# Optimization experiments

Hardware: AMD Instinct MI355X
Metric: run time of the kernel (lower is better)

The kernel has to match this reference:

```python
import jax, jax.numpy as jnp
import numpy as np

B, S, BD, AD, H, NITER = 16, 512, 768, 768, 12, 3  # batch, seq, bert_dim, attention_dim, heads, c_c_Attention_num
DH = AD // H
SCALE = float(np.sqrt(BD))  # note: original scales by sqrt(bert_dim), not head dim


def setup_inputs() -> dict:
    key = jax.random.key(0)
    ks = jax.random.split(key, 12)
    sd = 0.02
    return {
        "sequence1": jax.random.normal(ks[0], (B, S, BD), dtype=jnp.float32),
        "sequence2": jax.random.normal(ks[1], (B, S, BD), dtype=jnp.float32),
        # first-layer projections (bias=False), torch Linear weight layout [out, in]
        "Wq": jax.random.normal(ks[2], (AD, BD), dtype=jnp.float32) * sd,
        "Wk": jax.random.normal(ks[3], (AD, BD), dtype=jnp.float32) * sd,
        "Wv": jax.random.normal(ks[4], (AD, BD), dtype=jnp.float32) * sd,
        # later-layer projections (with bias), stacked over layer_num-1 = 2 layers
        "Wq1": jax.random.normal(ks[5], (2, AD, AD), dtype=jnp.float32) * sd,
        "bq1": jax.random.normal(ks[6], (2, AD), dtype=jnp.float32) * sd,
        "Wk1": jax.random.normal(ks[7], (2, AD, AD), dtype=jnp.float32) * sd,
        "bk1": jax.random.normal(ks[8], (2, AD), dtype=jnp.float32) * sd,
        "Wv1": jax.random.normal(ks[9], (2, AD, AD), dtype=jnp.float32) * sd,
        "bv1": jax.random.normal(ks[10], (2, AD), dtype=jnp.float32) * sd,
    }


def _attention(s1, s2, Wq, bq, Wk, bk, Wv, bv):
    # dropout is identity in eval mode
    q = s1 @ Wq.T + bq  # [B,S,AD]
    k = s2 @ Wk.T + bk
    v = s2 @ Wv.T + bv
    # torch.split along feature dim then stack on dim 0 == reshape to heads
    qh = q.reshape(B, S, H, DH)
    kh = k.reshape(B, S, H, DH)
    vh = v.reshape(B, S, H, DH)
    scores = jnp.einsum("bqhd,bkhd->hbqk", qh, kh)  # [H,B,S,S]
    scores = jax.nn.softmax(jnp.tanh(scores) / SCALE, axis=3)
    ctx = jnp.einsum("hbqk,bkhd->bqhd", scores, vh).reshape(B, S, AD)
    return ctx, scores


def reference(sequence1, sequence2, Wq, Wk, Wv, Wq1, bq1, Wk1, bk1, Wv1, bv1):
    s1, s2 = sequence1, sequence2
    ctx, sc = None, None
    for i in range(NITER):
        if i == 0:
            ctx, sc = _attention(s1, s2, Wq, 0.0, Wk, 0.0, Wv, 0.0)
        else:
            j = i - 1
            ctx, sc = _attention(s1, s2, Wq1[j], bq1[j], Wk1[j], bk1[j], Wv1[j], bv1[j])
        s1 = ctx
        s2 = ctx
    return ctx, ctx, sc
```

## Files before the change

### kernel.cpp

```cpp
#include <hip/hip_runtime.h>
#include <stdint.h>

typedef unsigned short u16;
typedef unsigned int u32;

typedef __bf16 bf16x8 __attribute__((ext_vector_type(8)));
typedef float f32x4 __attribute__((ext_vector_type(4)));

#define NQ 6291456
#define NW 589824
#define INV_SCALE 0.03608439182435161f
#define LOG2E2 2.885390081777927f

__device__ __forceinline__ u16 f2bf(float f) {
    u32 u = __float_as_uint(f);
    u32 r = (u + 0x7fffu + ((u >> 16) & 1u)) >> 16;
    return (u16)r;
}

__device__ __forceinline__ float score_p(float s) {
    float e  = exp2f(LOG2E2 * s);
    float th = 1.f - __fdividef(2.f, e + 1.f);
    float a  = th * INV_SCALE;
    return fmaf(a, fmaf(a, fmaf(a, 0.16666667f, 0.5f), 1.f), 1.f);
}

__device__ __forceinline__ void gload_lds16(const void* g, void* l) {
    __builtin_amdgcn_global_load_lds(
        (const __attribute__((address_space(1))) char*)(uintptr_t)g,
        (__attribute__((address_space(3))) char*)(uintptr_t)l, 16, 0, 0);
}

__device__ __forceinline__ f32x4 mfma16(bf16x8 a, bf16x8 b, f32x4 c) {
    return __builtin_amdgcn_mfma_f32_16x16x32_bf16(a, b, c, 0, 0, 0);
}

#define LDS_FENCE() asm volatile("s_waitcnt lgkmcnt(0)" ::: "memory")

struct CvtArgs {
    const float* src[8];
    u16* dst[8];
    int blk_start[8];
    int n4[8];
};

__global__ __launch_bounds__(256) void cvt_multi(CvtArgs a)
{
    const int bid = blockIdx.x;
    int seg = 0;
#pragma unroll
    for (int s = 1; s < 8; ++s) seg += (bid >= a.blk_start[s]);
    const int i = (bid - a.blk_start[seg]) * 256 + threadIdx.x;
    if (i < a.n4[seg]) {
        float4 v = ((const float4*)a.src[seg])[i];
        ushort4 o;
        o.x = f2bf(v.x); o.y = f2bf(v.y); o.z = f2bf(v.z); o.w = f2bf(v.w);
        ((ushort4*)a.dst[seg])[i] = o;
    }
}

__global__ __launch_bounds__(256, 2) void proj_gemm(
    const u16* __restrict__ A0, const u16* __restrict__ A1,
    const u16* __restrict__ Wq, const u16* __restrict__ Wk, const u16* __restrict__ Wv,
    const float* __restrict__ bq, const float* __restrict__ bk, const float* __restrict__ bv,
    u16* __restrict__ oq, u16* __restrict__ ok, u16* __restrict__ ov)
{
    __shared__ u16 sA[2][8192];
    __shared__ u16 sB[2][8192];

    const int z = blockIdx.z;
    const u16* A       = (z == 0) ? A0 : A1;
    const u16* W       = (z == 0) ? Wq : ((z == 1) ? Wk : Wv);
    const float* bias  = (z == 0) ? bq : ((z == 1) ? bk : bv);
    u16* out           = (z == 0) ? oq : ((z == 1) ? ok : ov);

    const int tid = threadIdx.x;
    const int wave = tid >> 6, lane = tid & 63;
    const int m0 = blockIdx.x * 128, n0 = blockIdx.y * 128;
    const int wrow = wave >> 1, wcol = wave & 1;
    const int lr = lane & 15, lg = lane >> 4;

    const int Lb0 = wave * 4096;
    const int srow = (Lb0 + lane * 16) >> 7;
    const int ssl = (lane & 7);

    f32x4 acc[4][4];
#pragma unroll
    for (int mi = 0; mi < 4; ++mi)
#pragma unroll
        for (int ni = 0; ni < 4; ++ni)
            acc[mi][ni] = (f32x4){0.f, 0.f, 0.f, 0.f};

#define STAGE(buf, k0)                                                          \
    {                                                                           \
        _Pragma("unroll")                                                       \
        for (int i = 0; i < 4; ++i) {                                           \
            const int row = srow + i * 8;                                       \
            const int sc16 = ssl ^ (row & 7);                                   \
            gload_lds16(A + (size_t)(m0 + row) * 768 + (k0) + sc16 * 8,         \
                        (char*)sA[buf] + Lb0 + i * 1024);                       \
            gload_lds16(W + (size_t)(n0 + row) * 768 + (k0) + sc16 * 8,         \
                        (char*)sB[buf] + Lb0 + i * 1024);                       \
        }                                                                       \
    }

    STAGE(0, 0);
    __syncthreads();

    for (int ks = 0; ks < 12; ++ks) {
        const int cur = ks & 1;
        if (ks < 11) STAGE(cur ^ 1, (ks + 1) * 64);
#pragma unroll
        for (int kk = 0; kk < 2; ++kk) {
            bf16x8 af[4], bfr[4];
#pragma unroll
            for (int t = 0; t < 4; ++t) {
                const int ar = wrow * 64 + t * 16 + lr;
                const int ac = (kk * 4 + lg) ^ (ar & 7);
                af[t] = *(const bf16x8*)((const char*)sA[cur] + ar * 128 + ac * 16);
                const int br = wcol * 64 + t * 16 + lr;
                const int bc = (kk * 4 + lg) ^ (br & 7);
                bfr[t] = *(const bf16x8*)((const char*)sB[cur] + br * 128 + bc * 16);
            }
#pragma unroll
            for (int mi = 0; mi < 4; ++mi)
#pragma unroll
                for (int ni = 0; ni < 4; ++ni)
                    acc[mi][ni] = mfma16(af[mi], bfr[ni], acc[mi][ni]);
        }
        __syncthreads();
    }
#undef STAGE

    float bvv[4] = {0.f, 0.f, 0.f, 0.f};
    if (bias) {
#pragma unroll
        for (int ni = 0; ni < 4; ++ni)
            bvv[ni] = bias[n0 + wcol * 64 + ni * 16 + lr];
    }
#pragma unroll
    for (int mi = 0; mi < 4; ++mi) {
#pragma unroll
        for (int ni = 0; ni < 4; ++ni) {
#pragma unroll
            for (int r = 0; r < 4; ++r) {
                const int rowM = m0 + wrow * 64 + mi * 16 + lg * 4 + r;
                const int colN = n0 + wcol * 64 + ni * 16 + lr;
                out[(size_t)rowM * 768 + colN] = f2bf(acc[mi][ni][r] + bvv[ni]);
            }
        }
    }
}

__global__ __launch_bounds__(256) void vtrans(const u16* __restrict__ v, u16* __restrict__ vT)
{
    __shared__ u16 t[64][80];
    const int blk = blockIdx.x;
    const int b = blk / 96, h = (blk / 8) % 12, st = blk & 7;
    const int tid = threadIdx.x;

    const u16* src = v + (size_t)(b * 512 + st * 64) * 768 + h * 64;
#pragma unroll
    for (int p = 0; p < 2; ++p) {
        const int srow = p * 32 + (tid >> 3), dp = tid & 7;
        uint4 d = *(const uint4*)(src + (size_t)srow * 768 + dp * 8);
        *(uint4*)&t[srow][dp * 8] = d;
    }
    __syncthreads();
    u16* dst = vT + (size_t)((b * 12 + h) * 64) * 512 + st * 64;
#pragma unroll
    for (int p = 0; p < 2; ++p) {
        const int drow = p * 32 + (tid >> 3), sp = tid & 7;
        union { u16 u[8]; uint4 v4; } o;
#pragma unroll
        for (int j = 0; j < 8; ++j) o.u[j] = t[sp * 8 + j][drow];
        *(uint4*)(dst + (size_t)drow * 512 + sp * 8) = o.v4;
    }
}

__global__ __launch_bounds__(256, 4) void attn_stream(
    const u16* __restrict__ q, const u16* __restrict__ k, const u16* __restrict__ vT,
    u16* __restrict__ ctx)
{
    __shared__ u16 sS[4][2][640];

    const int blk = blockIdx.x;
    const int b = blk / 96, h = (blk / 8) % 12, qc = blk & 7;
    const int tid = threadIdx.x, wave = tid >> 6, lane = tid & 63;
    const int q0 = qc * 64 + wave * 16;
    const int lr = lane & 15, lg = lane >> 4;

    const u16* qbase = q + (size_t)(b * 512 + q0 + lr) * 768 + h * 64 + lg * 8;
    bf16x8 aq0 = *(const bf16x8*)(qbase);
    bf16x8 aq1 = *(const bf16x8*)(qbase + 32);

    const u16* kbase = k + (size_t)(b * 512 + lr) * 768 + h * 64 + lg * 8;
    const u16* vbase = vT + (size_t)((b * 12 + h) * 64 + lr) * 512 + lg * 8;

    char* const myS0 = (char*)sS[wave][0];
    const int rdoff = lr * 80 + ((lg * 16) ^ ((lr & 3) << 4));

    float psum[4] = {0.f, 0.f, 0.f, 0.f};
    f32x4 o[4];
#pragma unroll
    for (int dt = 0; dt < 4; ++dt) o[dt] = (f32x4){0.f, 0.f, 0.f, 0.f};

    for (int w = 0; w < 16; ++w) {
        char* myS = myS0 + (w & 1) * 1280;
        const u16* kb = kbase + (size_t)w * 32 * 768;
        f32x4 s4a = (f32x4){0.f, 0.f, 0.f, 0.f};
        f32x4 s4b = (f32x4){0.f, 0.f, 0.f, 0.f};
        s4a = mfma16(aq0, *(const bf16x8*)kb, s4a);
        s4a = mfma16(aq1, *(const bf16x8*)(kb + 32), s4a);
        const u16* kb2 = kb + 16 * 768;
        s4b = mfma16(aq0, *(const bf16x8*)kb2, s4b);
        s4b = mfma16(aq1, *(const bf16x8*)(kb2 + 32), s4b);

#pragma unroll
        for (int c = 0; c < 2; ++c) {
#pragma unroll
            for (int r = 0; r < 4; ++r) {
                const float s = c ? s4b[r] : s4a[r];
                const float p = score_p(s);
                psum[r] += p;
                const int row = lg * 4 + r;
                const int byte = row * 80 + (((c * 16 + lr) * 2) ^ ((r & 3) << 4));
                *(u16*)(myS + byte) = f2bf(p);
            }
        }
        LDS_FENCE();
        bf16x8 pa = *(const bf16x8*)(myS + rdoff);
#pragma unroll
        for (int dt = 0; dt < 4; ++dt) {
            bf16x8 vb = *(const bf16x8*)(vbase + (size_t)dt * 16 * 512 + w * 32);
            o[dt] = mfma16(pa, vb, o[dt]);
        }
    }

#pragma unroll
    for (int r = 0; r < 4; ++r) {
        psum[r] += __shfl_xor(psum[r], 1);
        psum[r] += __shfl_xor(psum[r], 2);
        psum[r] += __shfl_xor(psum[r], 4);
        psum[r] += __shfl_xor(psum[r], 8);
    }
    float inv[4];
#pragma unroll
    for (int r = 0; r < 4; ++r) inv[r] = 1.f / psum[r];

#pragma unroll
    for (int dt = 0; dt < 4; ++dt) {
#pragma unroll
        for (int r = 0; r < 4; ++r) {
            const size_t gi = (size_t)(b * 512 + q0 + lg * 4 + r) * 768 + h * 64 + dt * 16 + lr;
            ctx[gi] = f2bf(o[dt][r] * inv[r]);
        }
    }
}

__global__ __launch_bounds__(256, 2) void attn_final(
    const u16* __restrict__ q, const u16* __restrict__ k, const u16* __restrict__ vT,
    float* __restrict__ ctxf, float* __restrict__ sc)
{
    __shared__ u16 sP[4][8192];
    __shared__ float ssum[4][16];

    const int blk = blockIdx.x;
    const int b = blk / 96, h = (blk / 8) % 12, qc = blk & 7;
    const int tid = threadIdx.x, wave = tid >> 6, lane = tid & 63;
    const int q0 = qc * 64 + wave * 16;
    const int lr = lane & 15, lg = lane >> 4;
    char* myP = (char*)sP[wave];

    const u16* qbase = q + (size_t)(b * 512 + q0 + lr) * 768 + h * 64 + lg * 8;
    bf16x8 aq0 = *(const bf16x8*)(qbase);
    bf16x8 aq1 = *(const bf16x8*)(qbase + 32);

    float psum[4] = {0.f, 0.f, 0.f, 0.f};
    const u16* kbase = k + (size_t)(b * 512 + lr) * 768 + h * 64 + lg * 8;

    for (int kt = 0; kt < 32; ++kt) {
        f32x4 s4 = (f32x4){0.f, 0.f, 0.f, 0.f};
        const u16* kb = kbase + (size_t)kt * 16 * 768;
        s4 = mfma16(aq0, *(const bf16x8*)kb, s4);
        s4 = mfma16(aq1, *(const bf16x8*)(kb + 32), s4);
#pragma unroll
        for (int r = 0; r < 4; ++r) {
            const int row = lg * 4 + r;
            const float p = score_p(s4[r]);
            psum[r] += p;
            const int byte = (row * 1024 + (kt * 16 + lr) * 2) ^ ((row & 7) << 4);
            *(u16*)(myP + byte) = f2bf(p);
        }
    }
#pragma unroll
    for (int r = 0; r < 4; ++r) {
        psum[r] += __shfl_xor(psum[r], 1);
        psum[r] += __shfl_xor(psum[r], 2);
        psum[r] += __shfl_xor(psum[r], 4);
        psum[r] += __shfl_xor(psum[r], 8);
    }
    float inv[4];
#pragma unroll
    for (int r = 0; r < 4; ++r) inv[r] = 1.f / psum[r];

    if (lr == 0) {
#pragma unroll
        for (int r = 0; r < 4; ++r) ssum[wave][lg * 4 + r] = inv[r];
    }

    const u16* vb0 = vT + (size_t)((b * 12 + h) * 64 + lr) * 512 + lg * 8;
#pragma unroll
    for (int dt = 0; dt < 4; ++dt) {
        f32x4 o = (f32x4){0.f, 0.f, 0.f, 0.f};
        const u16* vbb = vb0 + (size_t)dt * 16 * 512;
#pragma unroll
        for (int pk = 0; pk < 16; ++pk) {
            const int byte = (lr * 1024 + pk * 64 + lg * 16) ^ ((lr & 7) << 4);
            bf16x8 pa = *(const bf16x8*)(myP + byte);
            bf16x8 vb = *(const bf16x8*)(vbb + pk * 32);
            o = mfma16(pa, vb, o);
        }
#pragma unroll
        for (int r = 0; r < 4; ++r) {
            const float val = o[r] * inv[r];
            const size_t gi = (size_t)(b * 512 + q0 + lg * 4 + r) * 768 + h * 64 + dt * 16 + lr;
            ctxf[gi] = val;
            ctxf[gi + (size_t)NQ] = val;
        }
    }

#pragma unroll
    for (int row = 0; row < 16; ++row) {
        const float is = ssum[wave][row];
        const int byte = (row * 1024 + lane * 16) ^ ((row & 7) << 4);
        bf16x8 pv8 = *(const bf16x8*)(myP + byte);
        float4 o0, o1;
        o0.x = (float)pv8[0] * is; o0.y = (float)pv8[1] * is;
        o0.z = (float)pv8[2] * is; o0.w = (float)pv8[3] * is;
        o1.x = (float)pv8[4] * is; o1.y = (float)pv8[5] * is;
        o1.z = (float)pv8[6] * is; o1.w = (float)pv8[7] * is;
        float* dstp = sc + ((size_t)((h * 16 + b) * 512 + q0 + row)) * 512 + lane * 8;
        *(float4*)dstp = o0;
        *(float4*)(dstp + 4) = o1;
    }
}

extern "C" void kernel_launch(void* const* d_in, const int* in_sizes, int n_in,
                              void* d_out, int out_size, void* d_ws, size_t ws_size,
                              hipStream_t stream)
{
    if (n_in < 11) return;
    const float* seq1 = (const float*)d_in[0];
    const float* seq2 = (const float*)d_in[1];
    const float* Wq  = (const float*)d_in[2];
    const float* Wk  = (const float*)d_in[3];
    const float* Wv  = (const float*)d_in[4];
    const float* Wq1 = (const float*)d_in[5];
    const float* bq1 = (const float*)d_in[6];
    const float* Wk1 = (const float*)d_in[7];
    const float* bk1 = (const float*)d_in[8];
    const float* Wv1 = (const float*)d_in[9];
    const float* bv1 = (const float*)d_in[10];

    if (ws_size < ((size_t)7 * NQ + 9 * NW) * 2) return;
    u16* ws   = (u16*)d_ws;
    u16* q    = ws;
    u16* kk   = ws + (size_t)NQ;
    u16* vv   = ws + (size_t)2 * NQ;
    u16* vT   = ws + (size_t)3 * NQ;
    u16* ctx  = ws + (size_t)4 * NQ;
    u16* bs1  = ws + (size_t)5 * NQ;
    u16* bs2  = ws + (size_t)6 * NQ;
    u16* bWq  = ws + (size_t)7 * NQ;
    u16* bWk  = bWq  + (size_t)NW;
    u16* bWv  = bWk  + (size_t)NW;
    u16* bWq1 = bWv  + (size_t)NW;
    u16* bWk1 = bWq1 + (size_t)2 * NW;
    u16* bWv1 = bWk1 + (size_t)2 * NW;

    float* out = (float*)d_out;

    CvtArgs ca;
    const float* srcs[8] = {seq1, seq2, Wq, Wk, Wv, Wq1, Wk1, Wv1};
    u16* dsts[8] = {bs1, bs2, bWq, bWk, bWv, bWq1, bWk1, bWv1};
    const int n4s[8] = {NQ/4, NQ/4, NW/4, NW/4, NW/4, NW/2, NW/2, NW/2};
    int acc_blk = 0;
    for (int s = 0; s < 8; ++s) {
        ca.src[s] = srcs[s]; ca.dst[s] = dsts[s]; ca.n4[s] = n4s[s];
        ca.blk_start[s] = acc_blk;
        acc_blk += (n4s[s] + 255) / 256;
    }
    cvt_multi<<<acc_blk, 256, 0, stream>>>(ca);

    dim3 pgrid(64, 6, 3);

    proj_gemm<<<pgrid, 256, 0, stream>>>(bs1, bs2, bWq, bWk, bWv,
                                         nullptr, nullptr, nullptr, q, kk, vv);
    vtrans<<<1536, 256, 0, stream>>>(vv, vT);
    attn_stream<<<1536, 256, 0, stream>>>(q, kk, vT, ctx);

    proj_gemm<<<pgrid, 256, 0, stream>>>(ctx, ctx, bWq1, bWk1, bWv1,
                                         bq1, bk1, bv1, q, kk, vv);
    vtrans<<<1536, 256, 0, stream>>>(vv, vT);
    attn_stream<<<1536, 256, 0, stream>>>(q, kk, vT, ctx);

    proj_gemm<<<pgrid, 256, 0, stream>>>(ctx, ctx, bWq1 + (size_t)NW, bWk1 + (size_t)NW,
                                         bWv1 + (size_t)NW,
                                         bq1 + 768, bk1 + 768, bv1 + 768, q, kk, vv);
    vtrans<<<1536, 256, 0, stream>>>(vv, vT);
    attn_final<<<1536, 256, 0, stream>>>(q, kk, vT, out, out + (size_t)2 * NQ);
}
```

Before: 452.6 us.

## Recompute scores in two passes for final attention, streaming probabilities directly

The final attention kernel no longer holds the full 16x512 bf16 probability tile per wave in LDS. It makes one pass to get row sums, then a second pass that recomputes QK^T, writes the normalized fp32 scores straight to global memory, and streams P through a small double-buffered LDS tile into the PV MFMAs. This cuts LDS use enough to allow 4 blocks per SM, at the cost of recomputing the scores and tanh/exp. Both attention kernels also change block indexing so that consecutive blocks cover different batch-head pairs, which changes L2 locality. Scores are now written as 16-lane scalar rows instead of float4 vectors, which may hurt write coalescing.

```diff
diff --git a/kernel.cpp b/kernel.cpp
--- a/kernel.cpp
+++ b/kernel.cpp
@@ -185,7 +185,8 @@
     __shared__ u16 sS[4][2][640];
 
     const int blk = blockIdx.x;
-    const int b = blk / 96, h = (blk / 8) % 12, qc = blk & 7;
+    const int bh = blk % 192, qc = blk / 192;
+    const int b = bh / 12, h = bh % 12;
     const int tid = threadIdx.x, wave = tid >> 6, lane = tid & 63;
     const int q0 = qc * 64 + wave * 16;
     const int lr = lane & 15, lg = lane >> 4;
@@ -258,40 +259,42 @@
     }
 }
 
-__global__ __launch_bounds__(256, 2) void attn_final(
+__global__ __launch_bounds__(256, 4) void attn_final(
     const u16* __restrict__ q, const u16* __restrict__ k, const u16* __restrict__ vT,
     float* __restrict__ ctxf, float* __restrict__ sc)
 {
-    __shared__ u16 sP[4][8192];
-    __shared__ float ssum[4][16];
+    __shared__ u16 sS[4][2][640];
 
     const int blk = blockIdx.x;
-    const int b = blk / 96, h = (blk / 8) % 12, qc = blk & 7;
+    const int bh = blk % 192, qc = blk / 192;
+    const int b = bh / 12, h = bh % 12;
     const int tid = threadIdx.x, wave = tid >> 6, lane = tid & 63;
     const int q0 = qc * 64 + wave * 16;
     const int lr = lane & 15, lg = lane >> 4;
-    char* myP = (char*)sP[wave];
 
     const u16* qbase = q + (size_t)(b * 512 + q0 + lr) * 768 + h * 64 + lg * 8;
     bf16x8 aq0 = *(const bf16x8*)(qbase);
     bf16x8 aq1 = *(const bf16x8*)(qbase + 32);
 
+    const u16* kbase = k + (size_t)(b * 512 + lr) * 768 + h * 64 + lg * 8;
+    const u16* vbase = vT + (size_t)((b * 12 + h) * 64 + lr) * 512 + lg * 8;
+
+    char* const myS0 = (char*)sS[wave][0];
+    const int rdoff = lr * 80 + ((lg * 16) ^ ((lr & 3) << 4));
+
     float psum[4] = {0.f, 0.f, 0.f, 0.f};
-    const u16* kbase = k + (size_t)(b * 512 + lr) * 768 + h * 64 + lg * 8;
-
-    for (int kt = 0; kt < 32; ++kt) {
-        f32x4 s4 = (f32x4){0.f, 0.f, 0.f, 0.f};
-        const u16* kb = kbase + (size_t)kt * 16 * 768;
-        s4 = mfma16(aq0, *(const bf16x8*)kb, s4);
-        s4 = mfma16(aq1, *(const bf16x8*)(kb + 32), s4);
-#pragma unroll
-        for (int r = 0; r < 4; ++r) {
-            const int row = lg * 4 + r;
-            const float p = score_p(s4[r]);
-            psum[r] += p;
-            const int byte = (row * 1024 + (kt * 16 + lr) * 2) ^ ((row & 7) << 4);
-            *(u16*)(myP + byte) = f2bf(p);
-        }
+    for (int w = 0; w < 16; ++w) {
+        const u16* kb = kbase + (size_t)w * 32 * 768;
+        f32x4 s4a = (f32x4){0.f, 0.f, 0.f, 0.f};
+        f32x4 s4b = (f32x4){0.f, 0.f, 0.f, 0.f};
+        s4a = mfma16(aq0, *(const bf16x8*)kb, s4a);
+        s4a = mfma16(aq1, *(const bf16x8*)(kb + 32), s4a);
+        const u16* kb2 = kb + 16 * 768;
+        s4b = mfma16(aq0, *(const bf16x8*)kb2, s4b);
+        s4b = mfma16(aq1, *(const bf16x8*)(kb2 + 32), s4b);
+#pragma unroll
+        for (int r = 0; r < 4; ++r)
+            psum[r] += score_p(s4a[r]) + score_p(s4b[r]);
     }
 #pragma unroll
     for (int r = 0; r < 4; ++r) {
@@ -304,45 +307,53 @@
 #pragma unroll
     for (int r = 0; r < 4; ++r) inv[r] = 1.f / psum[r];
 
-    if (lr == 0) {
-#pragma unroll
-        for (int r = 0; r < 4; ++r) ssum[wave][lg * 4 + r] = inv[r];
-    }
-
-    const u16* vb0 = vT + (size_t)((b * 12 + h) * 64 + lr) * 512 + lg * 8;
+    f32x4 o[4];
+#pragma unroll
+    for (int dt = 0; dt < 4; ++dt) o[dt] = (f32x4){0.f, 0.f, 0.f, 0.f};
+
+    float* scb = sc + ((size_t)((h * 16 + b) * 512 + q0)) * 512;
+
+    for (int w = 0; w < 16; ++w) {
+        char* myS = myS0 + (w & 1) * 1280;
+        const u16* kb = kbase + (size_t)w * 32 * 768;
+        f32x4 s4a = (f32x4){0.f, 0.f, 0.f, 0.f};
+        f32x4 s4b = (f32x4){0.f, 0.f, 0.f, 0.f};
+        s4a = mfma16(aq0, *(const bf16x8*)kb, s4a);
+        s4a = mfma16(aq1, *(const bf16x8*)(kb + 32), s4a);
+        const u16* kb2 = kb + 16 * 768;
+        s4b = mfma16(aq0, *(const bf16x8*)kb2, s4b);
+        s4b = mfma16(aq1, *(const bf16x8*)(kb2 + 32), s4b);
+
+#pragma unroll
+        for (int c = 0; c < 2; ++c) {
+#pragma unroll
+            for (int r = 0; r < 4; ++r) {
+                const float s = c ? s4b[r] : s4a[r];
+                const float p = score_p(s);
+                const int row = lg * 4 + r;
+                scb[(size_t)row * 512 + w * 32 + c * 16 + lr] = p * inv[r];
+                const int byte = row * 80 + (((c * 16 + lr) * 2) ^ ((r & 3) << 4));
+                *(u16*)(myS + byte) = f2bf(p);
+            }
+        }
+        LDS_FENCE();
+        bf16x8 pa = *(const bf16x8*)(myS + rdoff);
+#pragma unroll
+        for (int dt = 0; dt < 4; ++dt) {
+            bf16x8 vb = *(const bf16x8*)(vbase + (size_t)dt * 16 * 512 + w * 32);
+            o[dt] = mfma16(pa, vb, o[dt]);
+        }
+    }
+
 #pragma unroll
     for (int dt = 0; dt < 4; ++dt) {
-        f32x4 o = (f32x4){0.f, 0.f, 0.f, 0.f};
-        const u16* vbb = vb0 + (size_t)dt * 16 * 512;
-#pragma unroll
-        for (int pk = 0; pk < 16; ++pk) {
-            const int byte = (lr * 1024 + pk * 64 + lg * 16) ^ ((lr & 7) << 4);
-            bf16x8 pa = *(const bf16x8*)(myP + byte);
-            bf16x8 vb = *(const bf16x8*)(vbb + pk * 32);
-            o = mfma16(pa, vb, o);
-        }
 #pragma unroll
         for (int r = 0; r < 4; ++r) {
-            const float val = o[r] * inv[r];
+            const float val = o[dt][r] * inv[r];
             const size_t gi = (size_t)(b * 512 + q0 + lg * 4 + r) * 768 + h * 64 + dt * 16 + lr;
             ctxf[gi] = val;
             ctxf[gi + (size_t)NQ] = val;
         }
-    }
-
-#pragma unroll
-    for (int row = 0; row < 16; ++row) {
-        const float is = ssum[wave][row];
-        const int byte = (row * 1024 + lane * 16) ^ ((row & 7) << 4);
-        bf16x8 pv8 = *(const bf16x8*)(myP + byte);
-        float4 o0, o1;
-        o0.x = (float)pv8[0] * is; o0.y = (float)pv8[1] * is;
-        o0.z = (float)pv8[2] * is; o0.w = (float)pv8[3] * is;
-        o1.x = (float)pv8[4] * is; o1.y = (float)pv8[5] * is;
-        o1.z = (float)pv8[6] * is; o1.w = (float)pv8[7] * is;
-        float* dstp = sc + ((size_t)((h * 16 + b) * 512 + q0 + row)) * 512 + lane * 8;
-        *(float4*)dstp = o0;
-        *(float4*)(dstp + 4) = o1;
     }
 }
 
```

New measurement: 473.7 us. 4.7% more time.
